# Kernel optimization log

Hardware: AMD Instinct MI355X
Metric: run time of the kernel (lower is better)

## Reference

```python
import jax, jax.numpy as jnp
from jax import lax
import numpy as np

DIM = 96
DINNER = 2 * DIM      # mamba expand=2
DSTATE = 16
DCONV = 4
DTRANK = 6            # ceil(DIM/16)
BN_EPS = 1e-5
LN_EPS = 1e-6


def setup_inputs() -> dict:
    key = jax.random.key(0)
    ks = jax.random.split(key, 12)
    B, H, W = 4, 64, 64
    f = lambda k, s, sc=0.02: (jax.random.normal(k, s, dtype=jnp.float32) * sc)
    return {
        "x1": jax.random.normal(ks[0], (B, 2 * DIM, H, W), dtype=jnp.float32),
        "x2": jax.random.normal(ks[1], (B, DIM, H, W), dtype=jnp.float32),
        # grouped conv 3x3: groups=DIM, in_per_group=3 -> kernel [DIM,3,3,3]
        "conv_w": f(ks[2], (DIM, 3, 3, 3), 0.1),
        "conv_b": jnp.zeros((DIM,), jnp.float32),
        "bn_g": jnp.ones((DIM,), jnp.float32),
        "bn_b": jnp.zeros((DIM,), jnp.float32),
        "ln_g": jnp.ones((DIM,), jnp.float32),
        "ln_b": jnp.zeros((DIM,), jnp.float32),
        "in_proj_w": f(ks[3], (2 * DINNER, DIM)),
        # depthwise causal conv1d: kernel [DINNER,1,DCONV]
        "conv1d_w": f(ks[4], (DINNER, 1, DCONV), 0.1),
        "conv1d_b": jnp.zeros((DINNER,), jnp.float32),
        "x_proj_w": f(ks[5], (DTRANK + 2 * DSTATE, DINNER)),
        "dt_proj_w": f(ks[6], (DINNER, DTRANK), 0.1),
        "dt_proj_b": jnp.full((DINNER,), -4.6, jnp.float32),  # softplus ~ 0.01
        "A_log": jnp.log(jnp.tile(jnp.arange(1, DSTATE + 1, dtype=jnp.float32)[None, :], (DINNER, 1))),
        "D": jnp.ones((DINNER,), jnp.float32),
        "out_proj_w": f(ks[7], (DIM, DINNER)),
        # grouped 1x1 down conv: groups=DIM//2, in_per_group=2 -> [DIM//2,2,1,1]
        "down_w": f(ks[8], (DIM // 2, 2, 1, 1), 0.1),
    }


def reference(x1, x2, conv_w, conv_b, bn_g, bn_b, ln_g, ln_b, in_proj_w,
              conv1d_w, conv1d_b, x_proj_w, dt_proj_w, dt_proj_b, A_log, D,
              out_proj_w, down_w):
    Bsz, _, H, W = x1.shape
    L = H * W
    # grouped conv 3x3 + BatchNorm (training-mode batch stats)
    xc = jnp.concatenate([x1, x2], axis=1)                                  # [B,3*DIM,H,W]
    y = lax.conv_general_dilated(xc, conv_w, (1, 1), ((1, 1), (1, 1)),
                                 dimension_numbers=("NCHW", "OIHW", "NCHW"),
                                 feature_group_count=DIM) + conv_b[None, :, None, None]
    mu = y.mean(axis=(0, 2, 3))
    var = y.var(axis=(0, 2, 3))
    y = (y - mu[None, :, None, None]) * lax.rsqrt(var + BN_EPS)[None, :, None, None]
    y = y * bn_g[None, :, None, None] + bn_b[None, :, None, None]
    res = y.reshape(Bsz, DIM, L).transpose(0, 2, 1)                          # [B,L,DIM]

    # Block_mamba(x2, y): out = res + Mamba(LN(tokens(x2)))
    u = x2.reshape(Bsz, DIM, L).transpose(0, 2, 1)                           # [B,L,DIM]
    m = u.mean(-1, keepdims=True)
    v = u.var(-1, keepdims=True)
    un = (u - m) * lax.rsqrt(v + LN_EPS) * ln_g + ln_b

    xz = un @ in_proj_w.T                                                    # [B,L,2*DINNER]
    xs, z = jnp.split(xz, 2, axis=-1)
    xs = xs.transpose(0, 2, 1)                                               # [B,DINNER,L]
    xs = lax.conv_general_dilated(xs, conv1d_w, (1,), ((DCONV - 1, 0),),
                                  dimension_numbers=("NCH", "OIH", "NCH"),
                                  feature_group_count=DINNER) + conv1d_b[None, :, None]
    xs = jax.nn.silu(xs).transpose(0, 2, 1)                                  # [B,L,DINNER]

    dbl = xs @ x_proj_w.T
    dt_r = dbl[..., :DTRANK]
    Bm = dbl[..., DTRANK:DTRANK + DSTATE]                                    # [B,L,N]
    Cm = dbl[..., DTRANK + DSTATE:]                                          # [B,L,N]
    dt = jax.nn.softplus(dt_r @ dt_proj_w.T + dt_proj_b)                     # [B,L,DINNER]

    A = -jnp.exp(A_log)                                                      # [DINNER,N]
    dA = jnp.exp(dt[..., None] * A)                                          # [B,L,DINNER,N]
    dBx = dt[..., None] * Bm[:, :, None, :] * xs[..., None]                  # [B,L,DINNER,N]

    def step(h, inp):
        dAt, dBxt, Ct = inp
        h = dAt * h + dBxt                                                   # [B,DINNER,N]
        return h, jnp.einsum("bdn,bn->bd", h, Ct)

    h0 = jnp.zeros((Bsz, DINNER, DSTATE), xs.dtype)
    _, ys = lax.scan(step, h0, (dA.transpose(1, 0, 2, 3),
                                dBx.transpose(1, 0, 2, 3),
                                Cm.transpose(1, 0, 2)))
    yss = ys.transpose(1, 0, 2) + xs * D                                     # [B,L,DINNER]
    out = (yss * jax.nn.silu(z)) @ out_proj_w.T + res                        # [B,L,DIM]
    out = out.transpose(0, 2, 1).reshape(Bsz, DIM, H, W)

    # grouped 1x1 down conv -> [B,DIM//2,H,W]
    return lax.conv_general_dilated(out, down_w, (1, 1), ((0, 0), (0, 0)),
                                    dimension_numbers=("NCHW", "OIHW", "NCHW"),
                                    feature_group_count=DIM // 2)
```

## Files before the change

kernel.cpp:

```cpp
#include <hip/hip_runtime.h>
#include <math.h>

#define B_    4
#define DIM_  96
#define L_    4096
#define DI_   192
#define DS_   16
#define NCH_  256
#define CHL_  16
#define NSUP_ 16
#define SUPL_ 16

__global__ __launch_bounds__(256) void k1_conv_bn(
    const float* __restrict__ x1, const float* __restrict__ x2,
    const float* __restrict__ cw, const float* __restrict__ cb,
    float* __restrict__ y_raw, float* __restrict__ bnpsum, float* __restrict__ bnpsq)
{
    __shared__ float sm[3][6][66];
    int bid  = blockIdx.x;
    int tile = bid & 15;
    int c    = (bid >> 4) % 96;
    int b    = bid / (16 * 96);
    int i0   = tile * 4;
    int tid  = threadIdx.x;

    const float* src = (c < 64) ? x1 + ((size_t)(b * 192 + 3 * c)) * L_
                                : x2 + ((size_t)(b * 96 + (3 * c - 192))) * L_;

    for (int q = tid; q < 3 * 6 * 66; q += 256) {
        int g = q / 396, rem = q - g * 396;
        int r = rem / 66, col = rem - r * 66;
        int gi = i0 - 1 + r, gj = col - 1;
        float v = 0.f;
        if (gi >= 0 && gi < 64 && gj >= 0 && gj < 64)
            v = src[g * L_ + gi * 64 + gj];
        sm[g][r][col] = v;
    }
    const float* wp = cw + c * 27;
    __syncthreads();

    int ri = tid >> 6, j = tid & 63;
    float acc = cb[c];
    #pragma unroll
    for (int g = 0; g < 3; ++g)
        #pragma unroll
        for (int di = 0; di < 3; ++di)
            #pragma unroll
            for (int dj = 0; dj < 3; ++dj)
                acc += sm[g][ri + di][j + dj] * wp[(g * 3 + di) * 3 + dj];

    y_raw[((size_t)(b * 96 + c)) * L_ + i0 * 64 + tid] = acc;

    float s1 = acc, s2 = acc * acc;
    for (int m = 32; m; m >>= 1) { s1 += __shfl_down(s1, m); s2 += __shfl_down(s2, m); }
    __shared__ float ls1[4], ls2[4];
    int wid = threadIdx.x >> 6, lane = threadIdx.x & 63;
    if (lane == 0) { ls1[wid] = s1; ls2[wid] = s2; }
    __syncthreads();
    if (threadIdx.x == 0) {
        int slot = c * 64 + b * 16 + tile;
        bnpsum[slot] = ls1[0] + ls1[1] + ls1[2] + ls1[3];
        bnpsq [slot] = ls2[0] + ls2[1] + ls2[2] + ls2[3];
    }
}

__global__ __launch_bounds__(64) void k2_bn_fin(
    const float* __restrict__ bnpsum, const float* __restrict__ bnpsq,
    const float* __restrict__ bng, const float* __restrict__ bnb,
    const float* __restrict__ A_log,
    float* __restrict__ scale, float* __restrict__ shift, float* __restrict__ aN)
{
    int c = blockIdx.x, lane = threadIdx.x;
    float s1 = bnpsum[c * 64 + lane];
    float s2 = bnpsq [c * 64 + lane];
    for (int m = 32; m; m >>= 1) { s1 += __shfl_down(s1, m); s2 += __shfl_down(s2, m); }
    if (lane == 0) {
        float mean = s1 * (1.0f / 16384.0f);
        float var  = s2 * (1.0f / 16384.0f) - mean * mean;
        float rstd = rsqrtf(var + 1e-5f);
        float sc = bng[c] * rstd;
        scale[c] = sc;
        shift[c] = bnb[c] - mean * sc;
    }
    int g = c * 32 + lane;
    if (lane < 32) aN[g] = -__expf(A_log[g]);
}

__global__ __launch_bounds__(256) void k3_ln_inproj(
    const float* __restrict__ x2, const float* __restrict__ lng, const float* __restrict__ lnb,
    const float* __restrict__ Wip, float* __restrict__ xs_t, float* __restrict__ z_t)
{
    __shared__ float unT[96][68];
    __shared__ float wt [96][68];
    int tid  = threadIdx.x;
    int rb   = blockIdx.x & 255;
    int cb   = blockIdx.x >> 8;
    int b    = rb >> 6;
    int l0   = (rb & 63) * 64;
    int col0 = cb * 64;

    for (int q = tid; q < 96 * 64; q += 256) {
        int c = q >> 6, dl = q & 63;
        unT[c][dl] = x2[((size_t)(b * 96 + c)) * L_ + l0 + dl];
    }
    for (int q = tid; q < 64 * 96; q += 256) {
        int dc = q / 96, k = q - dc * 96;
        wt[k][dc] = Wip[(size_t)(col0 + dc) * 96 + k];
    }
    __syncthreads();

    {
        int dl = tid >> 2, part = tid & 3;
        int c0 = part * 24;
        float s = 0.f, ss = 0.f;
        #pragma unroll
        for (int c = 0; c < 24; ++c) { float v = unT[c0 + c][dl]; s += v; ss += v * v; }
        s += __shfl_xor(s, 1); ss += __shfl_xor(ss, 1);
        s += __shfl_xor(s, 2); ss += __shfl_xor(ss, 2);
        float mean = s * (1.0f / 96.0f);
        float rstd = rsqrtf(ss * (1.0f / 96.0f) - mean * mean + 1e-6f);
        #pragma unroll
        for (int c = 0; c < 24; ++c) {
            int cc = c0 + c;
            unT[cc][dl] = (unT[cc][dl] - mean) * rstd * lng[cc] + lnb[cc];
        }
    }
    __syncthreads();

    int ri = tid >> 4, cj = tid & 15;
    float acc[4][4];
    #pragma unroll
    for (int i = 0; i < 4; ++i)
        #pragma unroll
        for (int j = 0; j < 4; ++j) acc[i][j] = 0.f;

    #pragma unroll 8
    for (int k = 0; k < 96; ++k) {
        float4 av = *(const float4*)&unT[k][ri * 4];
        float4 bv = *(const float4*)&wt [k][cj * 4];
        acc[0][0] += av.x * bv.x; acc[0][1] += av.x * bv.y; acc[0][2] += av.x * bv.z; acc[0][3] += av.x * bv.w;
        acc[1][0] += av.y * bv.x; acc[1][1] += av.y * bv.y; acc[1][2] += av.y * bv.z; acc[1][3] += av.y * bv.w;
        acc[2][0] += av.z * bv.x; acc[2][1] += av.z * bv.y; acc[2][2] += av.z * bv.z; acc[2][3] += av.z * bv.w;
        acc[3][0] += av.w * bv.x; acc[3][1] += av.w * bv.y; acc[3][2] += av.w * bv.z; acc[3][3] += av.w * bv.w;
    }

    float* dst = (cb < 3) ? xs_t : z_t;
    int cofs   = (cb < 3) ? col0 : col0 - DI_;
    #pragma unroll
    for (int i = 0; i < 4; ++i) {
        size_t row = (size_t)b * L_ + l0 + ri * 4 + i;
        float4 v = make_float4(acc[i][0], acc[i][1], acc[i][2], acc[i][3]);
        *(float4*)&dst[row * DI_ + cofs + cj * 4] = v;
    }
}

__global__ __launch_bounds__(256) void k4_conv1d_xproj(
    const float* __restrict__ xs_t, const float* __restrict__ w1, const float* __restrict__ b1,
    const float* __restrict__ Wxp, const float* __restrict__ Wdt, const float* __restrict__ bdt,
    float* __restrict__ xss_t, float* __restrict__ dt_t,
    float* __restrict__ Bm, float* __restrict__ Cm)
{
    __shared__ float xc [192][21];
    __shared__ float xss[192][17];
    __shared__ float dbl[38][17];
    int bid = blockIdx.x;
    int lt  = bid & 255;
    int b   = bid >> 8;
    int l0  = lt * 16;
    int tid = threadIdx.x;

    for (int q = tid; q < 192 * 19; q += 256) {
        int t = q / 192, d = q - t * 192;
        int l = l0 - 3 + t;
        xc[d][t] = (l >= 0) ? xs_t[((size_t)b * L_ + l) * DI_ + d] : 0.f;
    }
    __syncthreads();

    for (int q = tid; q < 192 * 16; q += 256) {
        int t = q / 192, d = q - t * 192;
        float acc = b1[d];
        #pragma unroll
        for (int k = 0; k < 4; ++k) acc += xc[d][t + k] * w1[d * 4 + k];
        acc = acc / (1.f + __expf(-acc));
        xss[d][t] = acc;
        xss_t[((size_t)b * L_ + l0 + t) * DI_ + d] = acc;
    }
    __syncthreads();

    for (int q = tid; q < 38 * 16; q += 256) {
        int col = q >> 4, t = q & 15;
        const float* wr = Wxp + col * 192;
        float acc = 0.f;
        #pragma unroll 8
        for (int d = 0; d < 192; ++d) acc += xss[d][t] * wr[d];
        dbl[col][t] = acc;
    }
    __syncthreads();

    for (int q = tid; q < 192 * 16; q += 256) {
        int t = q / 192, d = q - t * 192;
        float acc = bdt[d];
        #pragma unroll
        for (int r = 0; r < 6; ++r) acc += dbl[r][t] * Wdt[d * 6 + r];
        acc = (acc > 20.f) ? acc : __logf(1.f + __expf(acc));
        dt_t[((size_t)b * L_ + l0 + t) * DI_ + d] = acc;
    }
    {
        int n = tid & 15, t = tid >> 4;
        Bm[((size_t)b * L_ + l0 + t) * 16 + n] = dbl[6 + n][t];
        Cm[((size_t)b * L_ + l0 + t) * 16 + n] = dbl[22 + n][t];
    }
}

__global__ __launch_bounds__(192) void k5_scan_partial(
    const float* __restrict__ dt_t, const float* __restrict__ xss_t, const float* __restrict__ Bm,
    const float* __restrict__ aN, float* __restrict__ hpart, float* __restrict__ Ssum)
{
    int d     = threadIdx.x;
    int chunk = blockIdx.x & (NCH_ - 1);
    int b     = blockIdx.x >> 8;

    float a[16];
    #pragma unroll
    for (int n = 0; n < 16; ++n) a[n] = aN[d * 16 + n];

    size_t lbase = (size_t)b * L_ + chunk * CHL_;
    const float* dtp = dt_t  + lbase * DI_ + d;
    const float* xsp = xss_t + lbase * DI_ + d;
    const float4* Bp = (const float4*)(Bm + lbase * 16);

    float h[16];
    #pragma unroll
    for (int n = 0; n < 16; ++n) h[n] = 0.f;
    float S = 0.f;

    #pragma unroll 4
    for (int i = 0; i < CHL_; ++i) {
        float dt = dtp[(size_t)i * DI_];
        float xv = xsp[(size_t)i * DI_];
        S += dt;
        float4 B0 = Bp[i * 4 + 0], B1 = Bp[i * 4 + 1], B2 = Bp[i * 4 + 2], B3 = Bp[i * 4 + 3];
        float Bv[16] = {B0.x, B0.y, B0.z, B0.w, B1.x, B1.y, B1.z, B1.w,
                        B2.x, B2.y, B2.z, B2.w, B3.x, B3.y, B3.z, B3.w};
        float dtx = dt * xv;
        #pragma unroll
        for (int n = 0; n < 16; ++n) {
            float dA = __expf(dt * a[n]);
            h[n] = dA * h[n] + dtx * Bv[n];
        }
    }

    int sidx = (chunk * B_ + b) * DI_ + d;
    float4* hp = (float4*)(hpart + (size_t)sidx * 16);
    #pragma unroll
    for (int k = 0; k < 4; ++k)
        hp[k] = make_float4(h[4*k], h[4*k+1], h[4*k+2], h[4*k+3]);
    Ssum[sidx] = S;
}

__global__ __launch_bounds__(256) void k6a_seg(
    const float* __restrict__ hpart, const float* __restrict__ Ssum, const float* __restrict__ aN,
    float* __restrict__ Pseg, float* __restrict__ Hseg)
{
    int s = blockIdx.x / 48;
    int j = (blockIdx.x % 48) * 256 + threadIdx.x;
    float a = aN[j % (DI_ * 16)];
    float H = 0.f, P = 1.f;
    #pragma unroll
    for (int k = 0; k < SUPL_; ++k) {
        int c = s * SUPL_ + k;
        float Pc = __expf(Ssum[c * (B_ * DI_) + (j >> 4)] * a);
        H = Pc * H + hpart[(size_t)c * (B_ * DI_ * 16) + j];
        P *= Pc;
    }
    Pseg[(size_t)s * 12288 + j] = P;
    Hseg[(size_t)s * 12288 + j] = H;
}

__global__ __launch_bounds__(256) void k6b_scan(
    const float* __restrict__ Pseg, const float* __restrict__ Hseg, float* __restrict__ H0sup)
{
    int j = blockIdx.x * 256 + threadIdx.x;
    float H = 0.f;
    #pragma unroll
    for (int s = 0; s < NSUP_; ++s) {
        size_t idx = (size_t)s * 12288 + j;
        H0sup[idx] = H;
        H = Pseg[idx] * H + Hseg[idx];
    }
}

__global__ __launch_bounds__(256) void k6c_apply(
    float* __restrict__ hpart, const float* __restrict__ Ssum, const float* __restrict__ aN,
    const float* __restrict__ H0sup)
{
    int s = blockIdx.x / 48;
    int j = (blockIdx.x % 48) * 256 + threadIdx.x;
    float a = aN[j % (DI_ * 16)];
    float H = H0sup[(size_t)s * 12288 + j];
    #pragma unroll
    for (int k = 0; k < SUPL_; ++k) {
        int c = s * SUPL_ + k;
        size_t idx = (size_t)c * (B_ * DI_ * 16) + j;
        float hp = hpart[idx];
        float Pc = __expf(Ssum[c * (B_ * DI_) + (j >> 4)] * a);
        hpart[idx] = H;
        H = Pc * H + hp;
    }
}

__global__ __launch_bounds__(192) void k7_scan_final(
    const float* __restrict__ dt_t, const float* __restrict__ xss_t, const float* __restrict__ Bm,
    const float* __restrict__ Cm, const float* __restrict__ z_t, const float* __restrict__ aN,
    const float* __restrict__ Dp, const float* __restrict__ H0, float* __restrict__ g_t)
{
    int d     = threadIdx.x;
    int chunk = blockIdx.x & (NCH_ - 1);
    int b     = blockIdx.x >> 8;

    float a[16];
    #pragma unroll
    for (int n = 0; n < 16; ++n) a[n] = aN[d * 16 + n];
    float Dv = Dp[d];

    size_t lbase = (size_t)b * L_ + chunk * CHL_;
    const float* dtp = dt_t  + lbase * DI_ + d;
    const float* xsp = xss_t + lbase * DI_ + d;
    const float* zp  = z_t   + lbase * DI_ + d;
    const float4* Bp = (const float4*)(Bm + lbase * 16);
    const float4* Cp = (const float4*)(Cm + lbase * 16);
    float* gp = g_t + lbase * DI_ + d;

    int sidx = (chunk * B_ + b) * DI_ + d;
    float h[16];
    {
        const float4* h0 = (const float4*)(H0 + (size_t)sidx * 16);
        float4 h0a = h0[0], h0b = h0[1], h0c = h0[2], h0d = h0[3];
        h[0]=h0a.x; h[1]=h0a.y; h[2]=h0a.z; h[3]=h0a.w;
        h[4]=h0b.x; h[5]=h0b.y; h[6]=h0b.z; h[7]=h0b.w;
        h[8]=h0c.x; h[9]=h0c.y; h[10]=h0c.z; h[11]=h0c.w;
        h[12]=h0d.x; h[13]=h0d.y; h[14]=h0d.z; h[15]=h0d.w;
    }

    #pragma unroll 4
    for (int i = 0; i < CHL_; ++i) {
        float dt = dtp[(size_t)i * DI_];
        float xv = xsp[(size_t)i * DI_];
        float zv = zp [(size_t)i * DI_];
        float4 B0 = Bp[i * 4 + 0], B1 = Bp[i * 4 + 1], B2 = Bp[i * 4 + 2], B3 = Bp[i * 4 + 3];
        float4 C0 = Cp[i * 4 + 0], C1 = Cp[i * 4 + 1], C2 = Cp[i * 4 + 2], C3 = Cp[i * 4 + 3];
        float Bv[16] = {B0.x, B0.y, B0.z, B0.w, B1.x, B1.y, B1.z, B1.w,
                        B2.x, B2.y, B2.z, B2.w, B3.x, B3.y, B3.z, B3.w};
        float Cv[16] = {C0.x, C0.y, C0.z, C0.w, C1.x, C1.y, C1.z, C1.w,
                        C2.x, C2.y, C2.z, C2.w, C3.x, C3.y, C3.z, C3.w};
        float dtx = dt * xv;
        float y0 = 0.f, y1 = 0.f, y2 = 0.f, y3 = 0.f;
        #pragma unroll
        for (int n = 0; n < 16; n += 4) {
            float dA0 = __expf(dt * a[n]);
            float dA1 = __expf(dt * a[n+1]);
            float dA2 = __expf(dt * a[n+2]);
            float dA3 = __expf(dt * a[n+3]);
            h[n]   = dA0 * h[n]   + dtx * Bv[n];
            h[n+1] = dA1 * h[n+1] + dtx * Bv[n+1];
            h[n+2] = dA2 * h[n+2] + dtx * Bv[n+2];
            h[n+3] = dA3 * h[n+3] + dtx * Bv[n+3];
            y0 += h[n]   * Cv[n];
            y1 += h[n+1] * Cv[n+1];
            y2 += h[n+2] * Cv[n+2];
            y3 += h[n+3] * Cv[n+3];
        }
        float y = (y0 + y1) + (y2 + y3);
        float sz = zv / (1.f + __expf(-zv));
        gp[(size_t)i * DI_] = (y + xv * Dv) * sz;
    }
}

__global__ __launch_bounds__(256) void k8_out(
    const float* __restrict__ g_t, const float* __restrict__ Wout,
    const float* __restrict__ y_raw, const float* __restrict__ scale, const float* __restrict__ shift,
    const float* __restrict__ dw, float* __restrict__ out)
{
    __shared__ float gT[96][68];
    __shared__ float wt[96][98];
    int tid = threadIdx.x;
    int rb  = blockIdx.x;
    int b   = rb >> 6;
    int l0  = (rb & 63) * 64;
    int ri  = tid >> 4, cj = tid & 15;

    float acc[4][6];
    #pragma unroll
    for (int i = 0; i < 4; ++i)
        #pragma unroll
        for (int j = 0; j < 6; ++j) acc[i][j] = 0.f;

    for (int kc = 0; kc < 2; ++kc) {
        int k0 = kc * 96;
        for (int q = tid; q < 64 * 96; q += 256) {
            int dl = q / 96, k = q - dl * 96;
            gT[k][dl] = g_t[((size_t)b * L_ + l0 + dl) * DI_ + k0 + k];
        }
        for (int q = tid; q < 96 * 96; q += 256) {
            int c = q / 96, k = q - c * 96;
            wt[k][c] = Wout[(size_t)c * DI_ + k0 + k];
        }
        __syncthreads();

        #pragma unroll 4
        for (int k = 0; k < 96; ++k) {
            float4 av = *(const float4*)&gT[k][ri * 4];
            float b0 = wt[k][cj*6+0], b1 = wt[k][cj*6+1], b2 = wt[k][cj*6+2];
            float b3 = wt[k][cj*6+3], b4 = wt[k][cj*6+4], b5 = wt[k][cj*6+5];
            acc[0][0] += av.x*b0; acc[0][1] += av.x*b1; acc[0][2] += av.x*b2;
            acc[0][3] += av.x*b3; acc[0][4] += av.x*b4; acc[0][5] += av.x*b5;
            acc[1][0] += av.y*b0; acc[1][1] += av.y*b1; acc[1][2] += av.y*b2;
            acc[1][3] += av.y*b3; acc[1][4] += av.y*b4; acc[1][5] += av.y*b5;
            acc[2][0] += av.z*b0; acc[2][1] += av.z*b1; acc[2][2] += av.z*b2;
            acc[2][3] += av.z*b3; acc[2][4] += av.z*b4; acc[2][5] += av.z*b5;
            acc[3][0] += av.w*b0; acc[3][1] += av.w*b1; acc[3][2] += av.w*b2;
            acc[3][3] += av.w*b3; acc[3][4] += av.w*b4; acc[3][5] += av.w*b5;
        }
        __syncthreads();
    }

    int c0t = cj * 6;
    float w0 = dw[c0t+0], w1 = dw[c0t+1], w2 = dw[c0t+2];
    float w3 = dw[c0t+3], w4 = dw[c0t+4], w5 = dw[c0t+5];
    float sc[6], sh[6];
    #pragma unroll
    for (int j = 0; j < 6; ++j) { sc[j] = scale[c0t+j]; sh[j] = shift[c0t+j]; }

    #pragma unroll
    for (int i = 0; i < 4; ++i) {
        int l = l0 + ri * 4 + i;
        float os[6];
        #pragma unroll
        for (int j = 0; j < 6; ++j) {
            float r = y_raw[((size_t)(b * 96 + c0t + j)) * L_ + l] * sc[j] + sh[j];
            os[j] = acc[i][j] + r;
        }
        int o0 = cj * 3;
        out[((size_t)(b * 48 + o0 + 0)) * L_ + l] = os[0]*w0 + os[1]*w1;
        out[((size_t)(b * 48 + o0 + 1)) * L_ + l] = os[2]*w2 + os[3]*w3;
        out[((size_t)(b * 48 + o0 + 2)) * L_ + l] = os[4]*w4 + os[5]*w5;
    }
}

extern "C" void kernel_launch(void* const* d_in, const int* in_sizes, int n_in,
                              void* d_out, int out_size, void* d_ws, size_t ws_size,
                              hipStream_t stream)
{
    const float* x1     = (const float*)d_in[0];
    const float* x2     = (const float*)d_in[1];
    const float* conv_w = (const float*)d_in[2];
    const float* conv_b = (const float*)d_in[3];
    const float* bn_g   = (const float*)d_in[4];
    const float* bn_b   = (const float*)d_in[5];
    const float* ln_g   = (const float*)d_in[6];
    const float* ln_b   = (const float*)d_in[7];
    const float* Wip    = (const float*)d_in[8];
    const float* w1     = (const float*)d_in[9];
    const float* b1     = (const float*)d_in[10];
    const float* Wxp    = (const float*)d_in[11];
    const float* Wdt    = (const float*)d_in[12];
    const float* bdt    = (const float*)d_in[13];
    const float* A_log  = (const float*)d_in[14];
    const float* Dp     = (const float*)d_in[15];
    const float* Wout   = (const float*)d_in[16];
    const float* dw     = (const float*)d_in[17];

    float* ws = (float*)d_ws;
    size_t o = 0;
    float* y_raw  = ws + o; o += (size_t)B_ * 96 * L_;
    float* bnpsum = ws + o; o += 96 * 64;
    float* bnpsq  = ws + o; o += 96 * 64;
    float* scale  = ws + o; o += 96;
    float* shift  = ws + o; o += 96;
    float* aN     = ws + o; o += DI_ * DS_;
    float* xs_t   = ws + o; o += (size_t)B_ * DI_ * L_;
    float* z_t    = ws + o; o += (size_t)B_ * DI_ * L_;
    float* xss_t  = ws + o; o += (size_t)B_ * DI_ * L_;
    float* dt_t   = ws + o; o += (size_t)B_ * DI_ * L_;
    float* Bm     = ws + o; o += (size_t)B_ * L_ * DS_;
    float* Cm     = ws + o; o += (size_t)B_ * L_ * DS_;
    float* hpart  = ws + o; o += (size_t)NCH_ * B_ * DI_ * DS_;
    float* Ssum   = ws + o; o += (size_t)NCH_ * B_ * DI_;
    float* Pseg   = ws + o; o += (size_t)NSUP_ * B_ * DI_ * DS_;
    float* Hseg   = ws + o; o += (size_t)NSUP_ * B_ * DI_ * DS_;
    float* H0sup  = ws + o; o += (size_t)NSUP_ * B_ * DI_ * DS_;
    float* g_t    = xs_t;

    k1_conv_bn<<<B_ * 96 * 16, 256, 0, stream>>>(x1, x2, conv_w, conv_b, y_raw, bnpsum, bnpsq);
    k2_bn_fin<<<96, 64, 0, stream>>>(bnpsum, bnpsq, bn_g, bn_b, A_log, scale, shift, aN);
    k3_ln_inproj<<<6 * 256, 256, 0, stream>>>(x2, ln_g, ln_b, Wip, xs_t, z_t);
    k4_conv1d_xproj<<<B_ * 256, 256, 0, stream>>>(xs_t, w1, b1, Wxp, Wdt, bdt, xss_t, dt_t, Bm, Cm);
    k5_scan_partial<<<B_ * NCH_, 192, 0, stream>>>(dt_t, xss_t, Bm, aN, hpart, Ssum);
    k6a_seg<<<NSUP_ * 48, 256, 0, stream>>>(hpart, Ssum, aN, Pseg, Hseg);
    k6b_scan<<<48, 256, 0, stream>>>(Pseg, Hseg, H0sup);
    k6c_apply<<<NSUP_ * 48, 256, 0, stream>>>(hpart, Ssum, aN, H0sup);
    k7_scan_final<<<B_ * NCH_, 192, 0, stream>>>(dt_t, xss_t, Bm, Cm, z_t, aN, Dp, hpart, g_t);
    k8_out<<<B_ * 64, 256, 0, stream>>>(g_t, Wout, y_raw, scale, shift, dw, (float*)d_out);
}
```

Baseline: 144.9 us.

## Fuse conv1d/x_proj kernel with chunk-partial scan and tile x_proj via shared memory

Merges the conv1d+x_proj kernel with the per-chunk partial scan, so the scan reads dt, xs and B from shared memory instead of reloading them from global memory in a separate launch. The x_proj matmul is also restructured: weights are staged in shared-memory tiles of 48 columns, and activations are transposed to allow float4 dot products. This removes one launch and a global round trip, at the cost of more shared memory per block and 64 threads idling during the scan phase.

```diff
diff --git a/kernel.cpp b/kernel.cpp
--- a/kernel.cpp
+++ b/kernel.cpp
@@ -154,15 +154,18 @@
     }
 }
 
-__global__ __launch_bounds__(256) void k4_conv1d_xproj(
+__global__ __launch_bounds__(256) void k45_conv_xproj_scan(
     const float* __restrict__ xs_t, const float* __restrict__ w1, const float* __restrict__ b1,
     const float* __restrict__ Wxp, const float* __restrict__ Wdt, const float* __restrict__ bdt,
+    const float* __restrict__ aN,
     float* __restrict__ xss_t, float* __restrict__ dt_t,
-    float* __restrict__ Bm, float* __restrict__ Cm)
+    float* __restrict__ Bm, float* __restrict__ Cm,
+    float* __restrict__ hpart, float* __restrict__ Ssum)
 {
     __shared__ float xc [192][21];
-    __shared__ float xss[192][17];
+    __shared__ float xsT[16][204];
     __shared__ float dbl[38][17];
+    __shared__ float wx [38][52];
     int bid = blockIdx.x;
     int lt  = bid & 255;
     int b   = bid >> 8;
@@ -182,18 +185,42 @@
         #pragma unroll
         for (int k = 0; k < 4; ++k) acc += xc[d][t + k] * w1[d * 4 + k];
         acc = acc / (1.f + __expf(-acc));
-        xss[d][t] = acc;
+        xsT[t][d] = acc;
         xss_t[((size_t)b * L_ + l0 + t) * DI_ + d] = acc;
     }
     __syncthreads();
 
-    for (int q = tid; q < 38 * 16; q += 256) {
-        int col = q >> 4, t = q & 15;
-        const float* wr = Wxp + col * 192;
-        float acc = 0.f;
-        #pragma unroll 8
-        for (int d = 0; d < 192; ++d) acc += xss[d][t] * wr[d];
-        dbl[col][t] = acc;
+    float xacc0 = 0.f, xacc1 = 0.f, xacc2 = 0.f;
+    for (int kc = 0; kc < 4; ++kc) {
+        for (int q = tid; q < 38 * 48; q += 256) {
+            int col = q / 48, k = q - col * 48;
+            wx[col][k] = Wxp[(size_t)col * 192 + kc * 48 + k];
+        }
+        __syncthreads();
+        #pragma unroll
+        for (int r = 0; r < 3; ++r) {
+            int q = tid + r * 256;
+            if (q < 38 * 16) {
+                int col = q >> 4, t = q & 15;
+                float s = 0.f;
+                #pragma unroll
+                for (int d4 = 0; d4 < 12; ++d4) {
+                    float4 xv = *(const float4*)&xsT[t][kc * 48 + d4 * 4];
+                    float4 wv = *(const float4*)&wx [col][d4 * 4];
+                    s += xv.x * wv.x + xv.y * wv.y + xv.z * wv.z + xv.w * wv.w;
+                }
+                if (r == 0) xacc0 += s; else if (r == 1) xacc1 += s; else xacc2 += s;
+            }
+        }
+        __syncthreads();
+    }
+    #pragma unroll
+    for (int r = 0; r < 3; ++r) {
+        int q = tid + r * 256;
+        if (q < 38 * 16) {
+            int col = q >> 4, t = q & 15;
+            dbl[col][t] = (r == 0) ? xacc0 : (r == 1) ? xacc1 : xacc2;
+        }
     }
     __syncthreads();
 
@@ -204,58 +231,43 @@
         for (int r = 0; r < 6; ++r) acc += dbl[r][t] * Wdt[d * 6 + r];
         acc = (acc > 20.f) ? acc : __logf(1.f + __expf(acc));
         dt_t[((size_t)b * L_ + l0 + t) * DI_ + d] = acc;
+        xc[d][t] = acc;
     }
     {
         int n = tid & 15, t = tid >> 4;
         Bm[((size_t)b * L_ + l0 + t) * 16 + n] = dbl[6 + n][t];
         Cm[((size_t)b * L_ + l0 + t) * 16 + n] = dbl[22 + n][t];
     }
-}
-
-__global__ __launch_bounds__(192) void k5_scan_partial(
-    const float* __restrict__ dt_t, const float* __restrict__ xss_t, const float* __restrict__ Bm,
-    const float* __restrict__ aN, float* __restrict__ hpart, float* __restrict__ Ssum)
-{
-    int d     = threadIdx.x;
-    int chunk = blockIdx.x & (NCH_ - 1);
-    int b     = blockIdx.x >> 8;
-
-    float a[16];
-    #pragma unroll
-    for (int n = 0; n < 16; ++n) a[n] = aN[d * 16 + n];
-
-    size_t lbase = (size_t)b * L_ + chunk * CHL_;
-    const float* dtp = dt_t  + lbase * DI_ + d;
-    const float* xsp = xss_t + lbase * DI_ + d;
-    const float4* Bp = (const float4*)(Bm + lbase * 16);
-
-    float h[16];
-    #pragma unroll
-    for (int n = 0; n < 16; ++n) h[n] = 0.f;
-    float S = 0.f;
-
-    #pragma unroll 4
-    for (int i = 0; i < CHL_; ++i) {
-        float dt = dtp[(size_t)i * DI_];
-        float xv = xsp[(size_t)i * DI_];
-        S += dt;
-        float4 B0 = Bp[i * 4 + 0], B1 = Bp[i * 4 + 1], B2 = Bp[i * 4 + 2], B3 = Bp[i * 4 + 3];
-        float Bv[16] = {B0.x, B0.y, B0.z, B0.w, B1.x, B1.y, B1.z, B1.w,
-                        B2.x, B2.y, B2.z, B2.w, B3.x, B3.y, B3.z, B3.w};
-        float dtx = dt * xv;
-        #pragma unroll
-        for (int n = 0; n < 16; ++n) {
-            float dA = __expf(dt * a[n]);
-            h[n] = dA * h[n] + dtx * Bv[n];
-        }
-    }
-
-    int sidx = (chunk * B_ + b) * DI_ + d;
-    float4* hp = (float4*)(hpart + (size_t)sidx * 16);
-    #pragma unroll
-    for (int k = 0; k < 4; ++k)
-        hp[k] = make_float4(h[4*k], h[4*k+1], h[4*k+2], h[4*k+3]);
-    Ssum[sidx] = S;
+    __syncthreads();
+
+    if (tid < 192) {
+        int d = tid;
+        float a[16];
+        #pragma unroll
+        for (int n = 0; n < 16; ++n) a[n] = aN[d * 16 + n];
+        float h[16];
+        #pragma unroll
+        for (int n = 0; n < 16; ++n) h[n] = 0.f;
+        float S = 0.f;
+        #pragma unroll
+        for (int i = 0; i < CHL_; ++i) {
+            float dt = xc[d][i];
+            float xv = xsT[i][d];
+            float dtx = dt * xv;
+            S += dt;
+            #pragma unroll
+            for (int n = 0; n < 16; ++n) {
+                float dA = __expf(dt * a[n]);
+                h[n] = dA * h[n] + dtx * dbl[6 + n][i];
+            }
+        }
+        int sidx = (lt * B_ + b) * DI_ + d;
+        float4* hp = (float4*)(hpart + (size_t)sidx * 16);
+        #pragma unroll
+        for (int k = 0; k < 4; ++k)
+            hp[k] = make_float4(h[4*k], h[4*k+1], h[4*k+2], h[4*k+3]);
+        Ssum[sidx] = S;
+    }
 }
 
 __global__ __launch_bounds__(256) void k6a_seg(
@@ -494,8 +506,8 @@
     k1_conv_bn<<<B_ * 96 * 16, 256, 0, stream>>>(x1, x2, conv_w, conv_b, y_raw, bnpsum, bnpsq);
     k2_bn_fin<<<96, 64, 0, stream>>>(bnpsum, bnpsq, bn_g, bn_b, A_log, scale, shift, aN);
     k3_ln_inproj<<<6 * 256, 256, 0, stream>>>(x2, ln_g, ln_b, Wip, xs_t, z_t);
-    k4_conv1d_xproj<<<B_ * 256, 256, 0, stream>>>(xs_t, w1, b1, Wxp, Wdt, bdt, xss_t, dt_t, Bm, Cm);
-    k5_scan_partial<<<B_ * NCH_, 192, 0, stream>>>(dt_t, xss_t, Bm, aN, hpart, Ssum);
+    k45_conv_xproj_scan<<<B_ * 256, 256, 0, stream>>>(xs_t, w1, b1, Wxp, Wdt, bdt, aN,
+                                                      xss_t, dt_t, Bm, Cm, hpart, Ssum);
     k6a_seg<<<NSUP_ * 48, 256, 0, stream>>>(hpart, Ssum, aN, Pseg, Hseg);
     k6b_scan<<<48, 256, 0, stream>>>(Pseg, Hseg, H0sup);
     k6c_apply<<<NSUP_ * 48, 256, 0, stream>>>(hpart, Ssum, aN, H0sup);
```

New measurement: 156.4 us. 1.08x slower.
